# Optimization experiments

Hardware: AMD Instinct MI355X
Metric: run time of the kernel (lower is better)

The kernel has to match this reference:

```python
import jax, jax.numpy as jnp
import numpy as np


def setup_inputs() -> dict:
    key = jax.random.key(0)
    k1, k2, k3, k4, k5 = jax.random.split(key, 5)
    B, N, E, C_in, C_out, K = 64, 4096, 16, 64, 64, 3
    return {
        "x": jax.random.normal(k1, (B, N, C_in), dtype=jnp.float32),
        "adj_matrix": jax.random.normal(k2, (N, E), dtype=jnp.float32),
        "adj_embeddings": jax.random.normal(k3, (E, N), dtype=jnp.float32),
        "weights": jax.random.normal(k4, (K, C_in, C_out), dtype=jnp.float32) * 0.1,
        "bias": jax.random.normal(k5, (C_out,), dtype=jnp.float32) * 0.1,
    }


def reference(x, adj_matrix, adj_embeddings, weights, bias):
    # x: [B, N, C_in]; adj_matrix: [N, E]; adj_embeddings: [E, N]
    N = adj_matrix.shape[0]
    cheb_k = weights.shape[0]
    # adaptive adjacency: softmax(relu(adj @ emb), axis=1) -> [N, N]
    supports = jax.nn.softmax(jax.nn.relu(adj_matrix @ adj_embeddings), axis=1)
    # Chebyshev polynomial recursion: T0 = I, T1 = supports,
    # Tk = 2*supports @ T_{k-1} - T_{k-2}
    support_set = [jnp.eye(N, dtype=supports.dtype), supports]
    for _ in range(2, cheb_k):
        support_set.append(2.0 * supports @ support_set[-1] - support_set[-2])
    supports_k = jnp.stack(support_set, axis=0)  # [K, N, N]
    # aggregate: [K,N,M] x [B,M,C] -> [B,N,K,C]
    x_g = jnp.einsum("knm,bmc->bnkc", supports_k, x)
    # mix: [B,N,K,Cin] x [K,Cin,Cout] -> [B,N,Cout]
    return jnp.einsum("bnki,kio->bno", x_g, weights) + bias
```

## Files before the change

kernel.cpp:

```cpp
#include <hip/hip_runtime.h>


typedef __bf16 bf16;
typedef __bf16 bf16x8 __attribute__((ext_vector_type(8)));
typedef float f32x4 __attribute__((ext_vector_type(4)));

__device__ __forceinline__ void async_lds16(const void* g, void* l) {
  __builtin_amdgcn_global_load_lds((const __attribute__((address_space(1))) void*)g,
                                   (__attribute__((address_space(3))) void*)l, 16, 0, 0);
}

#define FENCE() asm volatile("" ::: "memory")
#define BAR()                          \
  do {                                 \
    FENCE();                           \
    __builtin_amdgcn_s_barrier();      \
    FENCE();                           \
  } while (0)
#define WAIT_VM(n) asm volatile("s_waitcnt vmcnt(" #n ")" ::: "memory")

__global__ __launch_bounds__(256) void build_wcat_k(const float* __restrict__ w, bf16* __restrict__ Wc) {
  int idx = blockIdx.x * 256 + threadIdx.x;
  if (idx >= 64 * 192) return;
  int o = idx / 192, kk = idx - o * 192;
  int k = kk >> 6, i = kk & 63;
  float v;
  if (k == 0)      v = w[i * 64 + o] - w[2 * 4096 + i * 64 + o];
  else if (k == 1) v = w[4096 + i * 64 + o];
  else             v = 2.f * w[2 * 4096 + i * 64 + o];
  Wc[idx] = (bf16)v;
}

__global__ __launch_bounds__(256) void supports_k(const float* __restrict__ adj,
                                                  const float* __restrict__ emb,
                                                  bf16* __restrict__ S) {
  __shared__ float slog[8][4096];
  __shared__ float sadj[8][16];
  __shared__ float swred[4][8];
  const int tid = threadIdx.x;
  const int lane = tid & 63, wv = tid >> 6;
  const int n0 = blockIdx.x * 8;
  if (tid < 128) sadj[tid >> 4][tid & 15] = adj[n0 * 16 + tid];
  __syncthreads();

  float mx[8];
  #pragma unroll
  for (int r = 0; r < 8; ++r) mx[r] = 0.f;

  for (int it = 0; it < 16; ++it) {
    const int j = it * 256 + tid;
    float e[16];
    #pragma unroll
    for (int k = 0; k < 16; ++k) e[k] = emb[k * 4096 + j];
    #pragma unroll
    for (int r = 0; r < 8; ++r) {
      float v = 0.f;
      #pragma unroll
      for (int k = 0; k < 16; ++k) v = fmaf(sadj[r][k], e[k], v);
      v = fmaxf(v, 0.f);
      slog[r][j] = v;
      mx[r] = fmaxf(mx[r], v);
    }
  }
  #pragma unroll
  for (int r = 0; r < 8; ++r) {
    #pragma unroll
    for (int off = 32; off > 0; off >>= 1) mx[r] = fmaxf(mx[r], __shfl_xor(mx[r], off, 64));
  }
  if (lane == 0) {
    #pragma unroll
    for (int r = 0; r < 8; ++r) swred[wv][r] = mx[r];
  }
  __syncthreads();
  #pragma unroll
  for (int r = 0; r < 8; ++r)
    mx[r] = fmaxf(fmaxf(swred[0][r], swred[1][r]), fmaxf(swred[2][r], swred[3][r]));

  float sm[8];
  #pragma unroll
  for (int r = 0; r < 8; ++r) sm[r] = 0.f;
  for (int it = 0; it < 16; ++it) {
    const int j = it * 256 + tid;
    #pragma unroll
    for (int r = 0; r < 8; ++r) {
      float ev = __expf(slog[r][j] - mx[r]);
      slog[r][j] = ev;
      sm[r] += ev;
    }
  }
  #pragma unroll
  for (int r = 0; r < 8; ++r) {
    #pragma unroll
    for (int off = 32; off > 0; off >>= 1) sm[r] += __shfl_xor(sm[r], off, 64);
  }
  __syncthreads();
  if (lane == 0) {
    #pragma unroll
    for (int r = 0; r < 8; ++r) swred[wv][r] = sm[r];
  }
  __syncthreads();
  float inv[8];
  #pragma unroll
  for (int r = 0; r < 8; ++r)
    inv[r] = 1.f / (swred[0][r] + swred[1][r] + swred[2][r] + swred[3][r]);

  for (int it = 0; it < 16; ++it) {
    const int j = it * 256 + tid;
    #pragma unroll
    for (int r = 0; r < 8; ++r)
      S[(n0 + r) * 4096 + j] = (bf16)(slog[r][j] * inv[r]);
  }
}

__global__ __launch_bounds__(256) void xpose_x_k(const float* __restrict__ x, bf16* __restrict__ Xt) {
  __shared__ float tile[64][65];
  const int tid = threadIdx.x;
  const int mt = blockIdx.x, b = blockIdx.y;
  const float* src = x + (b * 4096 + mt * 64) * 64;
  #pragma unroll
  for (int it = 0; it < 16; ++it) {
    const int idx = it * 256 + tid;
    tile[idx >> 6][idx & 63] = src[idx];
  }
  __syncthreads();
  #pragma unroll
  for (int it = 0; it < 16; ++it) {
    const int idx = it * 256 + tid;
    const int rr = idx >> 6, cc = idx & 63;
    Xt[(b * 64 + rr) * 4096 + mt * 64 + cc] = (bf16)tile[cc][rr];
  }
}

__global__ __launch_bounds__(256) void transpose_bf16_k(const bf16* __restrict__ in, bf16* __restrict__ outT) {
  __shared__ bf16 tile[64][65];
  const int tid = threadIdx.x;
  const int ti = blockIdx.x & 63, tj = blockIdx.x >> 6;
  #pragma unroll
  for (int it = 0; it < 16; ++it) {
    const int idx = it * 256 + tid;
    tile[idx >> 6][idx & 63] = in[(ti * 64 + (idx >> 6)) * 4096 + tj * 64 + (idx & 63)];
  }
  __syncthreads();
  #pragma unroll
  for (int it = 0; it < 16; ++it) {
    const int idx = it * 256 + tid;
    const int rr = idx >> 6, cc = idx & 63;
    outT[(tj * 64 + rr) * 4096 + ti * 64 + cc] = tile[cc][rr];
  }
}

__global__ __launch_bounds__(512, 2) void gemm256_k(const bf16* __restrict__ A,
                                                    const bf16* __restrict__ Bt,
                                                    bf16* __restrict__ C,
                                                    bf16* __restrict__ Ct) {
  __shared__ bf16 As[2][2][256][32];
  __shared__ bf16 Bs[2][2][256][32];

  const int tid = threadIdx.x;
  const int bid = blockIdx.x;
  const int wg = (bid & 7) * 32 + (bid >> 3);
  const int tm = wg >> 4, tn = wg & 15;
  const int rowBase = tm * 256, colBase = tn * 256;

  const int wv = tid >> 6, lane = tid & 63;
  const int wm = wv >> 2, wn = wv & 3;
  const int t16 = lane & 15, quad = lane >> 4;
  const int wv16 = wv * 16;
  const int q8 = (quad ^ ((t16 >> 1) & 3)) * 8;
  const int wm128 = wm * 128;
  const int wn64 = wn * 64;

  const int sr = tid >> 2;
  const int sc = ((tid & 3) ^ ((tid >> 3) & 3)) * 8;
  const bf16* gA = A + (size_t)(rowBase + sr) * 4096 + sc;
  const bf16* gB = Bt + (size_t)(colBase + sr) * 4096 + sc;

  f32x4 acc[8][4];
  #pragma unroll
  for (int i = 0; i < 8; ++i)
    #pragma unroll
    for (int j = 0; j < 4; ++j) acc[i][j] = (f32x4){0.f, 0.f, 0.f, 0.f};

  auto stA = [&](int buf, int s, int k0) {
    async_lds16(gA + k0 + s * 32, &As[buf][s][wv16][0]);
    async_lds16(gA + 524288 + k0 + s * 32, &As[buf][s][128 + wv16][0]);
  };
  auto stB = [&](int buf, int s, int k0) {
    async_lds16(gB + k0 + s * 32, &Bs[buf][s][wv16][0]);
    async_lds16(gB + 524288 + k0 + s * 32, &Bs[buf][s][128 + wv16][0]);
  };

  bf16x8 Ra[4], Rb[4], B0[4], B1[4];
  auto rdA = [&](bf16x8* R, int buf, int s, int g) {
    #pragma unroll
    for (int i = 0; i < 4; ++i)
      R[i] = *(const bf16x8*)&As[buf][s][wm128 + (g * 4 + i) * 16 + t16][q8];
  };
  auto rdB = [&](bf16x8* R, int buf, int s) {
    #pragma unroll
    for (int j = 0; j < 4; ++j)
      R[j] = *(const bf16x8*)&Bs[buf][s][wn64 + j * 16 + t16][q8];
  };
  auto mfma16 = [&](int g, const bf16x8* R, const bf16x8* Bv) {
    __builtin_amdgcn_s_setprio(1);
    #pragma unroll
    for (int i = 0; i < 4; ++i)
      #pragma unroll
      for (int j = 0; j < 4; ++j)
        acc[g * 4 + i][j] =
            __builtin_amdgcn_mfma_f32_16x16x32_bf16(R[i], Bv[j], acc[g * 4 + i][j], 0, 0, 0);
    __builtin_amdgcn_s_setprio(0);
  };

  stB(0, 0, 0); stA(0, 0, 0); stB(0, 1, 0); stA(0, 1, 0);
  stB(1, 0, 64); stA(1, 0, 64); stB(1, 1, 64);
  WAIT_VM(6);
  BAR();

  for (int it = 0; it < 31; ++it) {
    const int kb = it * 128;
    rdA(Ra, 0, 0, 0); rdB(B0, 0, 0); rdA(Rb, 0, 0, 1);
    stA(1, 1, kb + 64);
    mfma16(0, Ra, B0);
    BAR();
    rdA(Ra, 0, 1, 0); rdB(B1, 0, 1);
    stB(0, 0, kb + 128);
    mfma16(1, Rb, B0);
    BAR();
    rdA(Rb, 0, 1, 1);
    stA(0, 0, kb + 128);
    mfma16(0, Ra, B1);
    BAR();
    stB(0, 1, kb + 128);
    mfma16(1, Rb, B1);
    WAIT_VM(6);
    BAR();
    rdA(Ra, 1, 0, 0); rdB(B0, 1, 0); rdA(Rb, 1, 0, 1);
    stA(0, 1, kb + 128);
    mfma16(0, Ra, B0);
    BAR();
    rdA(Ra, 1, 1, 0); rdB(B1, 1, 1);
    stB(1, 0, kb + 192);
    mfma16(1, Rb, B0);
    BAR();
    rdA(Rb, 1, 1, 1);
    stA(1, 0, kb + 192);
    mfma16(0, Ra, B1);
    BAR();
    stB(1, 1, kb + 192);
    mfma16(1, Rb, B1);
    WAIT_VM(6);
    BAR();
  }

  rdA(Ra, 0, 0, 0); rdB(B0, 0, 0); rdA(Rb, 0, 0, 1);
  stA(1, 1, 4032);
  mfma16(0, Ra, B0);
  BAR();
  rdA(Ra, 0, 1, 0); rdB(B1, 0, 1);
  mfma16(1, Rb, B0);
  BAR();
  rdA(Rb, 0, 1, 1);
  mfma16(0, Ra, B1);
  BAR();
  mfma16(1, Rb, B1);
  WAIT_VM(0);
  BAR();
  rdA(Ra, 1, 0, 0); rdB(B0, 1, 0); rdA(Rb, 1, 0, 1);
  mfma16(0, Ra, B0);
  rdA(Ra, 1, 1, 0); rdB(B1, 1, 1);
  mfma16(1, Rb, B0);
  rdA(Rb, 1, 1, 1);
  mfma16(0, Ra, B1);
  mfma16(1, Rb, B1);

  #pragma unroll
  for (int i = 0; i < 8; ++i) {
    const int row0 = rowBase + wm128 + i * 16 + quad * 4;
    #pragma unroll
    for (int j = 0; j < 4; ++j) {
      const int col = colBase + wn64 + j * 16 + t16;
      #pragma unroll
      for (int rr = 0; rr < 4; ++rr)
        C[(size_t)(row0 + rr) * 4096 + col] = (bf16)acc[i][j][rr];
    }
  }
  if (Ct) {
    #pragma unroll
    for (int i = 0; i < 8; ++i) {
      const int row0 = rowBase + wm128 + i * 16 + quad * 4;
      #pragma unroll
      for (int j = 0; j < 4; ++j) {
        const int col = colBase + wn64 + j * 16 + t16;
        union { bf16 h[4]; uint2 u; } pk;
        #pragma unroll
        for (int rr = 0; rr < 4; ++rr) pk.h[rr] = (bf16)acc[i][j][rr];
        *(uint2*)(Ct + (size_t)col * 4096 + row0) = pk.u;
      }
    }
  }
}

__global__ __launch_bounds__(256) void mix_k(const float* __restrict__ x, const bf16* __restrict__ XG1,
                                             const bf16* __restrict__ XG2, const bf16* __restrict__ Wc,
                                             const float* __restrict__ bias, float* __restrict__ out) {
  __shared__ bf16 sW[64 * 200];
  const int tid = threadIdx.x;
  const int nt = blockIdx.x, b = blockIdx.y;
  {
    const int rw = tid >> 2, part = tid & 3;
    #pragma unroll
    for (int v = 0; v < 6; ++v)
      *(bf16x8*)(sW + rw * 200 + part * 48 + v * 8) = *(const bf16x8*)(Wc + rw * 192 + part * 48 + v * 8);
  }
  __syncthreads();

  const int lane = tid & 63, wv = tid >> 6;
  const int t16 = lane & 15, quad = lane >> 4;
  const int nBase = nt * 128 + wv * 32;

  f32x4 acc[2][4];
  #pragma unroll
  for (int i = 0; i < 2; ++i)
    #pragma unroll
    for (int j = 0; j < 4; ++j) acc[i][j] = (f32x4){0.f, 0.f, 0.f, 0.f};

  #pragma unroll
  for (int ch = 0; ch < 6; ++ch) {
    bf16x8 a[2];
    #pragma unroll
    for (int i = 0; i < 2; ++i) {
      const int row = nBase + i * 16 + t16;
      if (ch < 2) {
        const float* p = x + (b * 4096 + row) * 64 + ch * 32 + quad * 8;
        float4 f0 = *(const float4*)p;
        float4 f1 = *(const float4*)(p + 4);
        bf16x8 t;
        t[0] = (bf16)f0.x; t[1] = (bf16)f0.y; t[2] = (bf16)f0.z; t[3] = (bf16)f0.w;
        t[4] = (bf16)f1.x; t[5] = (bf16)f1.y; t[6] = (bf16)f1.z; t[7] = (bf16)f1.w;
        a[i] = t;
      } else {
        const bf16* src = (ch < 4) ? XG1 : XG2;
        a[i] = *(const bf16x8*)(src + row * 4096 + b * 64 + (ch & 1) * 32 + quad * 8);
      }
    }
    #pragma unroll
    for (int j = 0; j < 4; ++j) {
      bf16x8 wf = *(const bf16x8*)(sW + (j * 16 + t16) * 200 + ch * 32 + quad * 8);
      #pragma unroll
      for (int i = 0; i < 2; ++i)
        acc[i][j] = __builtin_amdgcn_mfma_f32_16x16x32_bf16(a[i], wf, acc[i][j], 0, 0, 0);
    }
  }

  #pragma unroll
  for (int j = 0; j < 4; ++j) {
    const float bb = bias[j * 16 + t16];
    #pragma unroll
    for (int i = 0; i < 2; ++i) {
      const int n0 = nBase + i * 16 + quad * 4;
      #pragma unroll
      for (int rr = 0; rr < 4; ++rr)
        out[(b * 4096 + n0 + rr) * 64 + j * 16 + t16] = acc[i][j][rr] + bb;
    }
  }
}

extern "C" void kernel_launch(void* const* d_in, const int* in_sizes, int n_in,
                              void* d_out, int out_size, void* d_ws, size_t ws_size,
                              hipStream_t stream) {
  const float* x    = (const float*)d_in[0];
  const float* adj  = (const float*)d_in[1];
  const float* emb  = (const float*)d_in[2];
  const float* w    = (const float*)d_in[3];
  const float* bias = (const float*)d_in[4];
  float* out = (float*)d_out;

  char* ws = (char*)d_ws;
  const size_t SZ = (size_t)4096 * 4096 * sizeof(bf16);
  bf16* S    = (bf16*)(ws);
  bf16* XG1  = (bf16*)(ws + SZ);
  bf16* XG2  = (bf16*)(ws + 2 * SZ);
  bf16* XBUF = (bf16*)(ws + 3 * SZ);
  const bool fused_t = ws_size >= 5 * SZ + (size_t)(64 * 192 * sizeof(bf16));
  bf16* XG1T = fused_t ? (bf16*)(ws + 4 * SZ) : XBUF;
  bf16* Wc   = (bf16*)(ws + (fused_t ? 5 : 4) * SZ);

  build_wcat_k<<<48, 256, 0, stream>>>(w, Wc);
  supports_k<<<512, 256, 0, stream>>>(adj, emb, S);
  xpose_x_k<<<dim3(64, 64), 256, 0, stream>>>(x, XBUF);
  gemm256_k<<<256, 512, 0, stream>>>(S, XBUF, XG1, fused_t ? XG1T : nullptr);
  if (!fused_t) transpose_bf16_k<<<4096, 256, 0, stream>>>(XG1, XBUF);
  gemm256_k<<<256, 512, 0, stream>>>(S, XG1T, XG2, nullptr);
  mix_k<<<dim3(32, 64), 256, 0, stream>>>(x, XG1, XG2, Wc, bias, out);
}
```

Before: 435.6 us.

## Fuse channel-mix epilogue into second Chebyshev GEMM, dropping XG2 buffer

The second S·XG1 GEMM no longer writes XG2 to global memory. Its accumulators are stashed as bf16 in the A/B shared-memory tiles, and each wave then runs the weight-mix MFMAs directly, reading x, XG1 and the stashed tile, adding bias and writing the output. This removes the separate mix kernel launch and a 32 MB bf16 write plus re-read. In exchange the GEMM epilogue gets longer, needs extra LDS for the weights (which may lower occupancy), and adds register pressure.

```diff
diff --git a/kernel.cpp b/kernel.cpp
--- a/kernel.cpp
+++ b/kernel.cpp
@@ -152,9 +152,14 @@
 __global__ __launch_bounds__(512, 2) void gemm256_k(const bf16* __restrict__ A,
                                                     const bf16* __restrict__ Bt,
                                                     bf16* __restrict__ C,
-                                                    bf16* __restrict__ Ct) {
+                                                    bf16* __restrict__ Ct,
+                                                    const float* __restrict__ xmix,
+                                                    const bf16* __restrict__ Wc,
+                                                    const float* __restrict__ bias,
+                                                    float* __restrict__ out) {
   __shared__ bf16 As[2][2][256][32];
   __shared__ bf16 Bs[2][2][256][32];
+  __shared__ bf16 sW[64 * 200];
 
   const int tid = threadIdx.x;
   const int bid = blockIdx.x;
@@ -169,6 +174,13 @@
   const int q8 = (quad ^ ((t16 >> 1) & 3)) * 8;
   const int wm128 = wm * 128;
   const int wn64 = wn * 64;
+
+  if (xmix) {
+    const int rw = tid >> 3, part = tid & 7;
+    #pragma unroll
+    for (int v = 0; v < 3; ++v)
+      *(bf16x8*)(sW + rw * 200 + part * 24 + v * 8) = *(const bf16x8*)(Wc + rw * 192 + part * 24 + v * 8);
+  }
 
   const int sr = tid >> 2;
   const int sc = ((tid & 3) ^ ((tid >> 3) & 3)) * 8;
@@ -274,82 +286,93 @@
   mfma16(0, Ra, B1);
   mfma16(1, Rb, B1);
 
-  #pragma unroll
-  for (int i = 0; i < 8; ++i) {
-    const int row0 = rowBase + wm128 + i * 16 + quad * 4;
-    #pragma unroll
-    for (int j = 0; j < 4; ++j) {
-      const int col = colBase + wn64 + j * 16 + t16;
-      #pragma unroll
-      for (int rr = 0; rr < 4; ++rr)
-        C[(size_t)(row0 + rr) * 4096 + col] = (bf16)acc[i][j][rr];
-    }
-  }
-  if (Ct) {
+  if (!xmix) {
     #pragma unroll
     for (int i = 0; i < 8; ++i) {
       const int row0 = rowBase + wm128 + i * 16 + quad * 4;
       #pragma unroll
       for (int j = 0; j < 4; ++j) {
         const int col = colBase + wn64 + j * 16 + t16;
-        union { bf16 h[4]; uint2 u; } pk;
         #pragma unroll
-        for (int rr = 0; rr < 4; ++rr) pk.h[rr] = (bf16)acc[i][j][rr];
-        *(uint2*)(Ct + (size_t)col * 4096 + row0) = pk.u;
+        for (int rr = 0; rr < 4; ++rr)
+          C[(size_t)(row0 + rr) * 4096 + col] = (bf16)acc[i][j][rr];
       }
     }
-  }
-}
-
-__global__ __launch_bounds__(256) void mix_k(const float* __restrict__ x, const bf16* __restrict__ XG1,
-                                             const bf16* __restrict__ XG2, const bf16* __restrict__ Wc,
-                                             const float* __restrict__ bias, float* __restrict__ out) {
-  __shared__ bf16 sW[64 * 200];
-  const int tid = threadIdx.x;
-  const int nt = blockIdx.x, b = blockIdx.y;
-  {
-    const int rw = tid >> 2, part = tid & 3;
-    #pragma unroll
-    for (int v = 0; v < 6; ++v)
-      *(bf16x8*)(sW + rw * 200 + part * 48 + v * 8) = *(const bf16x8*)(Wc + rw * 192 + part * 48 + v * 8);
-  }
-  __syncthreads();
-
-  const int lane = tid & 63, wv = tid >> 6;
-  const int t16 = lane & 15, quad = lane >> 4;
-  const int nBase = nt * 128 + wv * 32;
-
-  f32x4 acc[2][4];
-  #pragma unroll
-  for (int i = 0; i < 2; ++i)
-    #pragma unroll
-    for (int j = 0; j < 4; ++j) acc[i][j] = (f32x4){0.f, 0.f, 0.f, 0.f};
+    if (Ct) {
+      #pragma unroll
+      for (int i = 0; i < 8; ++i) {
+        const int row0 = rowBase + wm128 + i * 16 + quad * 4;
+        #pragma unroll
+        for (int j = 0; j < 4; ++j) {
+          const int col = colBase + wn64 + j * 16 + t16;
+          union { bf16 h[4]; uint2 u; } pk;
+          #pragma unroll
+          for (int rr = 0; rr < 4; ++rr) pk.h[rr] = (bf16)acc[i][j][rr];
+          *(uint2*)(Ct + (size_t)col * 4096 + row0) = pk.u;
+        }
+      }
+    }
+    return;
+  }
+
+  BAR();
+  bf16* stash = (wv < 4) ? ((bf16*)As + wv * 8192) : ((bf16*)Bs + (wv - 4) * 8192);
+  #pragma unroll
+  for (int i = 0; i < 8; ++i) {
+    #pragma unroll
+    for (int j = 0; j < 4; ++j) {
+      #pragma unroll
+      for (int rr = 0; rr < 4; ++rr) {
+        const int row = i * 16 + quad * 4 + rr;
+        const int lc = j * 2 + (t16 >> 3);
+        stash[row * 64 + ((lc ^ (row & 7)) * 8) + (t16 & 7)] = (bf16)acc[i][j][rr];
+      }
+    }
+  }
+  const int b = tn * 4 + wn;
+  const int nrow0 = rowBase + wm128;
+
+  f32x4 macc[8][4];
+  #pragma unroll
+  for (int i = 0; i < 8; ++i)
+    #pragma unroll
+    for (int j = 0; j < 4; ++j) macc[i][j] = (f32x4){0.f, 0.f, 0.f, 0.f};
 
   #pragma unroll
   for (int ch = 0; ch < 6; ++ch) {
-    bf16x8 a[2];
-    #pragma unroll
-    for (int i = 0; i < 2; ++i) {
-      const int row = nBase + i * 16 + t16;
-      if (ch < 2) {
-        const float* p = x + (b * 4096 + row) * 64 + ch * 32 + quad * 8;
-        float4 f0 = *(const float4*)p;
-        float4 f1 = *(const float4*)(p + 4);
-        bf16x8 t;
-        t[0] = (bf16)f0.x; t[1] = (bf16)f0.y; t[2] = (bf16)f0.z; t[3] = (bf16)f0.w;
-        t[4] = (bf16)f1.x; t[5] = (bf16)f1.y; t[6] = (bf16)f1.z; t[7] = (bf16)f1.w;
-        a[i] = t;
-      } else {
-        const bf16* src = (ch < 4) ? XG1 : XG2;
-        a[i] = *(const bf16x8*)(src + row * 4096 + b * 64 + (ch & 1) * 32 + quad * 8);
+    bf16x8 wf[4];
+    #pragma unroll
+    for (int j = 0; j < 4; ++j)
+      wf[j] = *(const bf16x8*)(sW + (j * 16 + t16) * 200 + ch * 32 + quad * 8);
+    #pragma unroll
+    for (int h = 0; h < 2; ++h) {
+      bf16x8 a4[4];
+      #pragma unroll
+      for (int ii = 0; ii < 4; ++ii) {
+        const int i = h * 4 + ii;
+        const int rl = i * 16 + t16;
+        const int rg = nrow0 + rl;
+        if (ch < 2) {
+          const float* p = xmix + ((size_t)(b * 4096 + rg)) * 64 + ch * 32 + quad * 8;
+          float4 f0 = *(const float4*)p;
+          float4 f1 = *(const float4*)(p + 4);
+          bf16x8 t;
+          t[0] = (bf16)f0.x; t[1] = (bf16)f0.y; t[2] = (bf16)f0.z; t[3] = (bf16)f0.w;
+          t[4] = (bf16)f1.x; t[5] = (bf16)f1.y; t[6] = (bf16)f1.z; t[7] = (bf16)f1.w;
+          a4[ii] = t;
+        } else if (ch < 4) {
+          a4[ii] = *(const bf16x8*)(C  + (size_t)rg * 4096 + b * 64 + (ch & 1) * 32 + quad * 8);
+        } else {
+          const int c = (ch & 1) * 4 + quad;
+          a4[ii] = *(const bf16x8*)(stash + rl * 64 + ((c ^ (rl & 7)) * 8));
+        }
       }
-    }
-    #pragma unroll
-    for (int j = 0; j < 4; ++j) {
-      bf16x8 wf = *(const bf16x8*)(sW + (j * 16 + t16) * 200 + ch * 32 + quad * 8);
-      #pragma unroll
-      for (int i = 0; i < 2; ++i)
-        acc[i][j] = __builtin_amdgcn_mfma_f32_16x16x32_bf16(a[i], wf, acc[i][j], 0, 0, 0);
+      #pragma unroll
+      for (int j = 0; j < 4; ++j)
+        #pragma unroll
+        for (int ii = 0; ii < 4; ++ii)
+          macc[h * 4 + ii][j] =
+              __builtin_amdgcn_mfma_f32_16x16x32_bf16(a4[ii], wf[j], macc[h * 4 + ii][j], 0, 0, 0);
     }
   }
 
@@ -357,11 +380,11 @@
   for (int j = 0; j < 4; ++j) {
     const float bb = bias[j * 16 + t16];
     #pragma unroll
-    for (int i = 0; i < 2; ++i) {
-      const int n0 = nBase + i * 16 + quad * 4;
+    for (int i = 0; i < 8; ++i) {
+      const int n0 = nrow0 + i * 16 + quad * 4;
       #pragma unroll
       for (int rr = 0; rr < 4; ++rr)
-        out[(b * 4096 + n0 + rr) * 64 + j * 16 + t16] = acc[i][j][rr] + bb;
+        out[((size_t)(b * 4096 + n0 + rr)) * 64 + j * 16 + t16] = macc[i][j][rr] + bb;
     }
   }
 }
@@ -380,7 +403,6 @@
   const size_t SZ = (size_t)4096 * 4096 * sizeof(bf16);
   bf16* S    = (bf16*)(ws);
   bf16* XG1  = (bf16*)(ws + SZ);
-  bf16* XG2  = (bf16*)(ws + 2 * SZ);
   bf16* XBUF = (bf16*)(ws + 3 * SZ);
   const bool fused_t = ws_size >= 5 * SZ + (size_t)(64 * 192 * sizeof(bf16));
   bf16* XG1T = fused_t ? (bf16*)(ws + 4 * SZ) : XBUF;
@@ -389,8 +411,9 @@
   build_wcat_k<<<48, 256, 0, stream>>>(w, Wc);
   supports_k<<<512, 256, 0, stream>>>(adj, emb, S);
   xpose_x_k<<<dim3(64, 64), 256, 0, stream>>>(x, XBUF);
-  gemm256_k<<<256, 512, 0, stream>>>(S, XBUF, XG1, fused_t ? XG1T : nullptr);
+  gemm256_k<<<256, 512, 0, stream>>>(S, XBUF, XG1, fused_t ? XG1T : nullptr,
+                                     nullptr, nullptr, nullptr, nullptr);
   if (!fused_t) transpose_bf16_k<<<4096, 256, 0, stream>>>(XG1, XBUF);
-  gemm256_k<<<256, 512, 0, stream>>>(S, XG1T, XG2, nullptr);
-  mix_k<<<dim3(32, 64), 256, 0, stream>>>(x, XG1, XG2, Wc, bias, out);
-}
+  gemm256_k<<<256, 512, 0, stream>>>(S, XG1T, XG1, nullptr,
+                                     x, Wc, bias, out);
+}
```

Measured after the change: 459.9 us. 1.06x slower.
